# Kernel optimization log

Measured on AMD Instinct MI355X. Metric: run time of the kernel, lower is better.

## Reference

```python
import jax, jax.numpy as jnp
import numpy as np

E = 16   # n_experts
K = 4    # top_k
NEG = jnp.float32(-1e20)


def _swiglu(x, w1, w2, w3):
    # bias-free SwiGLU expert: (swish(x@w1) * (x@w2)) @ w3
    a = x @ w1
    return (a * jax.nn.sigmoid(a) * (x @ w2)) @ w3


def setup_inputs() -> dict:
    key = jax.random.key(0)
    ks = jax.random.split(key, 9)
    B, S, D, H = 32, 512, 512, 1365  # H = D*2*4//3
    s = 0.02  # weight init scale to keep activations sane
    return {
        "x": jax.random.normal(ks[0], (B, S, D), jnp.float32),
        "gate_w": jax.random.normal(ks[1], (D, E), jnp.float32) * s,
        "routing_bias": jnp.zeros((E,), jnp.float32),
        "w1": jax.random.normal(ks[2], (E, D, H), jnp.float32) * s,
        "w2": jax.random.normal(ks[3], (E, D, H), jnp.float32) * s,
        "w3": jax.random.normal(ks[4], (E, H, D), jnp.float32) * s,
        "sw1": jax.random.normal(ks[5], (D, H), jnp.float32) * s,
        "sw2": jax.random.normal(ks[6], (D, H), jnp.float32) * s,
        "sw3": jax.random.normal(ks[7], (H, D), jnp.float32) * s,
    }


def reference(x, gate_w, routing_bias, w1, w2, w3, sw1, sw2, sw3):
    # gate logits + aux-free load-balancing bias  [B,S,E]
    gate_out = x @ gate_w + routing_bias
    top_v, top_i = jax.lax.top_k(gate_out, K)
    # chosen[b,s,e] = 1 if expert e is in the top-k for token (b,s)
    chosen = jax.nn.one_hot(top_i, E, dtype=x.dtype).sum(axis=-2)
    # scatter top-k values onto a -1e20 background, then softmax over experts
    masked = jnp.where(chosen > 0, gate_out, NEG)
    probs = jax.nn.softmax(masked, axis=-1)
    weights = probs * chosen  # zero outside the chosen set (matches torch mask)
    # shared expert runs on all tokens
    out = _swiglu(x, sw1, sw2, sw3)
    # per-expert SwiGLU, weighted-combined (loop over fixed small E)
    for e in range(E):
        out = out + _swiglu(x, w1[e], w2[e], w3[e]) * weights[..., e:e + 1]
    return out
```

## Files before the change

### kernel.cpp

```cpp
#include <hip/hip_runtime.h>

#define NT    16384
#define DDIM  512
#define HDIM  1365
#define HPAD  1408
#define NEXP  16
#define BK    64
#define MAXTILES 336
#define MAXSLOTS 86016

typedef unsigned short u16;
typedef unsigned int   u32;
typedef __attribute__((ext_vector_type(8))) __bf16 bf16x8;
typedef __attribute__((ext_vector_type(4))) float  f32x4;
typedef __attribute__((address_space(3))) void lds_void;
typedef __attribute__((address_space(1))) void glb_void;

__device__ __forceinline__ u16 f2bf(float f) {
  union { float f; u32 u; } v; v.f = f;
  u32 u = v.u;
  u += 0x7fffu + ((u >> 16) & 1u);
  return (u16)(u >> 16);
}

__device__ __forceinline__ float bf2f(u16 b) {
  union { u32 u; float f; } v; v.u = ((u32)b) << 16;
  return v.f;
}

__device__ __forceinline__ f32x4 mfma16(bf16x8 a, bf16x8 b, f32x4 c) {
  return __builtin_amdgcn_mfma_f32_16x16x32_bf16(a, b, c, 0, 0, 0);
}

__device__ __forceinline__ void gload16(const u16* g, u16* l) {
  __builtin_amdgcn_global_load_lds((const glb_void*)g, (lds_void*)l, 16, 0, 0);
}

__device__ __forceinline__ bf16x8 lds_frag(const u16* base, int row, int e0) {
  int b = ((row << 7) + (e0 << 1)) ^ ((row & 7) << 4);
  return *(const bf16x8*)((const char*)base + b);
}

__device__ __forceinline__ int swz_n(int bid, int n) {
  int q = n >> 3, r = n & 7;
  int xcd = bid & 7, j = bid >> 3;
  return (xcd < r ? xcd * (q + 1) : r * (q + 1) + (xcd - r) * q) + j;
}

__global__ void transpose12_kernel(const float* __restrict__ w1, const float* __restrict__ w2,
                                   const float* __restrict__ sw1, const float* __restrict__ sw2,
                                   u16* __restrict__ w1t, u16* __restrict__ w2t,
                                   u16* __restrict__ sw1t, u16* __restrict__ sw2t) {
  __shared__ float tile[32][65];
  int z = blockIdx.z;
  const float* in; u16* out;
  if (z < 16)      { in = w1 + (size_t)z * DDIM * HDIM;        out = w1t + (size_t)z * HPAD * DDIM; }
  else if (z < 32) { in = w2 + (size_t)(z - 16) * DDIM * HDIM; out = w2t + (size_t)(z - 16) * HPAD * DDIM; }
  else if (z == 32){ in = sw1; out = sw1t; }
  else             { in = sw2; out = sw2t; }
  int h0 = blockIdx.x * 32, d0 = blockIdx.y * 64;
  int tx = threadIdx.x, ty = threadIdx.y;
  int h = h0 + tx;
#pragma unroll
  for (int r = 0; r < 8; ++r) {
    int d = d0 + ty + r * 8;
    float v = (h < HDIM) ? in[(size_t)d * HDIM + h] : 0.f;
    tile[tx][ty + r * 8] = v;
  }
  __syncthreads();
#pragma unroll
  for (int r = 0; r < 4; ++r) {
    int hh = h0 + ty + r * 8;
    u32 lo = f2bf(tile[ty + r * 8][2 * tx]);
    u32 hi = f2bf(tile[ty + r * 8][2 * tx + 1]);
    ((u32*)&out[(size_t)hh * DDIM + d0])[tx] = lo | (hi << 16);
  }
}

__global__ void transpose3_kernel(const float* __restrict__ w3, const float* __restrict__ sw3,
                                  u16* __restrict__ w3t, u16* __restrict__ sw3t) {
  __shared__ float tile[32][65];
  int z = blockIdx.z;
  const float* in = (z < 16) ? (w3 + (size_t)z * HDIM * DDIM) : sw3;
  u16* out = (z < 16) ? (w3t + (size_t)z * DDIM * HPAD) : sw3t;
  int h0 = blockIdx.x * 64, d0 = blockIdx.y * 32;
  int tx = threadIdx.x, ty = threadIdx.y;
  int d = d0 + tx;
#pragma unroll
  for (int r = 0; r < 8; ++r) {
    int h = h0 + ty + r * 8;
    float v = (h < HDIM) ? in[(size_t)h * DDIM + d] : 0.f;
    tile[tx][ty + r * 8] = v;
  }
  __syncthreads();
#pragma unroll
  for (int r = 0; r < 4; ++r) {
    int dd = d0 + ty + r * 8;
    u32 lo = f2bf(tile[ty + r * 8][2 * tx]);
    u32 hi = f2bf(tile[ty + r * 8][2 * tx + 1]);
    ((u32*)&out[(size_t)dd * HPAD + h0])[tx] = lo | (hi << 16);
  }
}

__global__ __launch_bounds__(512) void routing_kernel(
    const float* __restrict__ x, const float* __restrict__ gw,
    const float* __restrict__ rbias, u16* __restrict__ x_bf,
    int* __restrict__ top_e, float* __restrict__ top_w) {
  __shared__ float gwp[NEXP * DDIM];
  int tid = threadIdx.x;
  for (int i = tid; i < NEXP * DDIM; i += 512) {
    int d = i >> 4, e = i & 15;
    gwp[e * DDIM + ((d & 7) << 6) + (d >> 3)] = gw[i];
  }
  __syncthreads();
  int w = tid >> 6, lane = tid & 63;
  int t = blockIdx.x * 8 + w;
  const float* xr = x + (size_t)t * DDIM + lane * 8;
  float4 xa = ((const float4*)xr)[0], xb = ((const float4*)xr)[1];
  float xv[8] = {xa.x, xa.y, xa.z, xa.w, xb.x, xb.y, xb.z, xb.w};
  u16 r[8];
#pragma unroll
  for (int k = 0; k < 8; ++k) r[k] = f2bf(xv[k]);
  *(uint4*)&x_bf[(size_t)t * DDIM + lane * 8] = *(const uint4*)r;
  float acc[NEXP];
#pragma unroll
  for (int e = 0; e < NEXP; ++e) {
    const float* ge = gwp + e * DDIM + lane;
    float s = 0.f;
#pragma unroll
    for (int k = 0; k < 8; ++k) s += xv[k] * ge[k << 6];
#pragma unroll
    for (int off = 32; off; off >>= 1) s += __shfl_xor(s, off);
    acc[e] = s + rbias[e];
  }
  if (lane == 0) {
    int sel[4]; float sv[4];
    unsigned used = 0;
#pragma unroll
    for (int i = 0; i < 4; ++i) {
      float best = -1e30f; int bi = 0;
#pragma unroll
      for (int e = 0; e < NEXP; ++e) {
        bool ok = !((used >> e) & 1u) && acc[e] > best;
        best = ok ? acc[e] : best;
        bi   = ok ? e : bi;
      }
      used |= 1u << bi; sel[i] = bi; sv[i] = best;
    }
    float m = sv[0];
    float ex[4]; float s = 0.f;
#pragma unroll
    for (int i = 0; i < 4; ++i) { ex[i] = __expf(sv[i] - m); s += ex[i]; }
    float inv = 1.f / s;
#pragma unroll
    for (int i = 0; i < 4; ++i) {
      top_e[t * 4 + i] = sel[i];
      top_w[t * 4 + i] = ex[i] * inv;
    }
  }
}

__global__ __launch_bounds__(1024) void rank_kernel(const int* __restrict__ top_e,
                                                    int* __restrict__ counts,
                                                    int* __restrict__ top_pos) {
  __shared__ int hist[NEXP], base[NEXP];
  int tid = threadIdx.x;
  int t = blockIdx.x * 1024 + tid;
  if (tid < NEXP) hist[tid] = 0;
  __syncthreads();
  int e4[4], r4[4];
#pragma unroll
  for (int i = 0; i < 4; ++i) {
    e4[i] = top_e[t * 4 + i];
    r4[i] = atomicAdd(&hist[e4[i]], 1);
  }
  __syncthreads();
  if (tid < NEXP) base[tid] = atomicAdd(&counts[tid], hist[tid]);
  __syncthreads();
#pragma unroll
  for (int i = 0; i < 4; ++i) top_pos[t * 4 + i] = base[e4[i]] + r4[i];
}

__global__ __launch_bounds__(256) void finish_kernel(
    const int* __restrict__ counts, const int* __restrict__ top_e,
    const float* __restrict__ top_w, const int* __restrict__ top_pos,
    int* __restrict__ slot_off, int* __restrict__ ntiles, int2* __restrict__ desc,
    int* __restrict__ tok_pad, float* __restrict__ w_pad, int* __restrict__ pos_list) {
  __shared__ int s_off[17], s_tb[17], s_nt[17], s_cnt[17];
  int tid = threadIdx.x;
  if (tid == 0) {
    int off = 0, td = 0;
    for (int e = 0; e < 17; ++e) {
      int c = (e == 16) ? NT : counts[e];
      s_cnt[e] = c; s_off[e] = off;
      int nt = (c + 255) >> 8;
      s_nt[e] = nt; s_tb[e] = td;
      td += nt; off += nt * 256;
    }
    if (blockIdx.x == 0) {
      for (int e = 0; e < 17; ++e) slot_off[e] = s_off[e];
      slot_off[17] = off;
      *ntiles = td;
    }
  }
  __syncthreads();
  if (blockIdx.x == 0) {
    for (int e = 0; e < 17; ++e)
      for (int i = tid; i < s_nt[e]; i += 256)
        desc[s_tb[e] + i] = make_int2(e, s_off[e] + i * 256);
  } else if (blockIdx.x == 1) {
    for (int e = 0; e < 16; ++e) {
      int c = s_cnt[e], padded = s_nt[e] * 256;
      for (int i = c + tid; i < padded; i += 256) {
        tok_pad[s_off[e] + i] = 0;
        w_pad[s_off[e] + i] = 0.f;
      }
    }
  }
  int t = blockIdx.x * 256 + tid;
#pragma unroll
  for (int i = 0; i < 4; ++i) {
    int e = top_e[t * 4 + i];
    int slot = s_off[e] + top_pos[t * 4 + i];
    tok_pad[slot] = t;
    w_pad[slot] = top_w[t * 4 + i];
    pos_list[t * 4 + i] = slot;
  }
  int sh = s_off[16] + t;
  tok_pad[sh] = t;
  w_pad[sh] = 1.f;
}

__global__ __launch_bounds__(512, 2) void gemm1_kernel(
    const u16* __restrict__ x_bf, const u16* __restrict__ w1t, const u16* __restrict__ w2t,
    const u16* __restrict__ sw1t, const u16* __restrict__ sw2t,
    const int* __restrict__ ntiles, const int2* __restrict__ desc,
    const int* __restrict__ tok_pad, u16* __restrict__ h, int lo, int ntc) {
  int wk = swz_n(blockIdx.x, ntc * 11);
  int tloc = wk / 11, hblk = wk - tloc * 11;
  int ti = (lo >> 8) + tloc;
  if (ti >= *ntiles) return;
  int2 de = desc[ti];
  int e = de.x, m0 = de.y;
  int n0h = hblk * 128;
  const u16* W1 = (e == 16) ? sw1t : (w1t + (size_t)e * HPAD * DDIM);
  const u16* W2 = (e == 16) ? sw2t : (w2t + (size_t)e * HPAD * DDIM);

  __shared__ u16 smem[65536];
  u16* As = smem;
  u16* Bs = smem + 32768;

  int tid = threadIdx.x, w = tid >> 6, lane = tid & 63;
  int wm = w >> 2, wn = w & 3, lr = lane & 15, lk = lane >> 4;

  const u16* ags[4]; const u16* bgs[4];
#pragma unroll
  for (int l = 0; l < 4; ++l) {
    int idx = l * 512 + tid;
    int row = idx >> 3, sl = idx & 7;
    int ce = ((sl ^ (row & 7)) << 3);
    ags[l] = x_bf + (size_t)tok_pad[m0 + row] * DDIM + ce;
    int grp = row >> 4;
    const u16* Wsrc = (grp & 1) ? W2 : W1;
    int hrow = n0h + ((grp >> 1) << 4) + (row & 15);
    bgs[l] = Wsrc + (size_t)hrow * DDIM + ce;
  }

  auto stage = [&](int kt, int buf) {
    int k0 = kt * BK;
#pragma unroll
    for (int l = 0; l < 4; ++l) {
      int db = buf * 16384 + l * 4096 + (w << 9);
      gload16(ags[l] + k0, As + db);
      gload16(bgs[l] + k0, Bs + db);
    }
  };

  f32x4 acc[8][4] = {};

  stage(0, 0);
  stage(1, 1);

  for (int t = 0; t < DDIM / BK; ++t) {
    int cur = t & 1;
    asm volatile("s_waitcnt vmcnt(8)" ::: "memory");
    __builtin_amdgcn_s_barrier();
    const u16* Ab = As + cur * 16384;
    const u16* Bb = Bs + cur * 16384;
#pragma unroll
    for (int kf = 0; kf < 2; ++kf) {
      int e0 = kf * 32 + lk * 8;
      bf16x8 bfr[4];
#pragma unroll
      for (int nf = 0; nf < 4; ++nf)
        bfr[nf] = lds_frag(Bb, wn * 64 + nf * 16 + lr, e0);
#pragma unroll
      for (int mf = 0; mf < 8; ++mf) {
        bf16x8 a = lds_frag(Ab, wm * 128 + mf * 16 + lr, e0);
#pragma unroll
        for (int nf = 0; nf < 4; ++nf)
          acc[mf][nf] = mfma16(a, bfr[nf], acc[mf][nf]);
      }
    }
    __builtin_amdgcn_s_barrier();
    int tn = (t + 2 < DDIM / BK) ? t + 2 : DDIM / BK - 1;
    stage(tn, cur);
  }
  asm volatile("s_waitcnt vmcnt(0)" ::: "memory");
  __builtin_amdgcn_s_barrier();

  u16* hs = smem;
#pragma unroll
  for (int mf = 0; mf < 8; ++mf)
#pragma unroll
    for (int hc = 0; hc < 2; ++hc)
#pragma unroll
      for (int j = 0; j < 4; ++j) {
        float g = acc[mf][hc * 2][j], u = acc[mf][hc * 2 + 1][j];
        float hv = g * u / (1.f + __expf(-g));
        int row = wm * 128 + mf * 16 + lk * 4 + j;
        int col = (wn * 2 + hc) * 16 + lr;
        hs[((row << 7) + col) ^ ((row & 7) << 3)] = f2bf(hv);
      }
  __syncthreads();
#pragma unroll
  for (int i = 0; i < 8; ++i) {
    int idx = (i * 512 + tid) * 8;
    int row = idx >> 7, col = idx & 127;
    *(uint4*)&h[(size_t)(m0 - lo + row) * HPAD + n0h + col] =
        *(uint4*)&hs[idx ^ ((row & 7) << 3)];
  }
}

template <bool YMODE>
__global__ __launch_bounds__(256, 3) void gemm2_kernel(
    const u16* __restrict__ h, const u16* __restrict__ w3t, const u16* __restrict__ sw3t,
    const int* __restrict__ ntiles, const int2* __restrict__ desc,
    const int* __restrict__ tok_pad, const float* __restrict__ w_pad,
    u16* __restrict__ y, float* __restrict__ out, int lo, int ntc) {
  int wk = swz_n(blockIdx.x, ntc * 8);
  int tloc = wk >> 3, sub = (wk >> 2) & 1, dblk = wk & 3;
  int ti = (lo >> 8) + tloc;
  if (ti >= *ntiles) return;
  int2 de = desc[ti];
  int e = de.x, m0 = de.y + sub * 128;
  int n0 = dblk * 128;
  const u16* W3 = (e == 16) ? sw3t : (w3t + (size_t)e * DDIM * HPAD);

  __shared__ u16 smem[16384];
  __shared__ float swl[128];
  u16* hs = smem;
  u16* ws3 = smem + 8192;

  int tid = threadIdx.x, w = tid >> 6, lane = tid & 63;
  int wm = w >> 1, wn = w & 1, lr = lane & 15, lk = lane >> 4;

  if (tid < 128) swl[tid] = w_pad[m0 + tid];

  const u16* ags[4]; const u16* bgs[4];
  int ce = (((lane & 7) ^ ((lane >> 3) & 7)) << 3);
#pragma unroll
  for (int p = 0; p < 4; ++p) {
    int r = w * 32 + p * 8 + (lane >> 3);
    ags[p] = h + (size_t)(m0 - lo + r) * HPAD + ce;
    bgs[p] = W3 + (size_t)(n0 + r) * HPAD + ce;
  }

  f32x4 acc[4][4] = {};

  for (int ks = 0; ks < HPAD / BK; ++ks) {
    int k0 = ks * BK;
#pragma unroll
    for (int p = 0; p < 4; ++p) {
      gload16(ags[p] + k0, hs + ((w * 32 + p * 8) << 6));
      gload16(bgs[p] + k0, ws3 + ((w * 32 + p * 8) << 6));
    }
    __syncthreads();
#pragma unroll
    for (int kf = 0; kf < 2; ++kf) {
      int e0 = kf * 32 + lk * 8;
      bf16x8 bfr[4];
#pragma unroll
      for (int nf = 0; nf < 4; ++nf)
        bfr[nf] = lds_frag(ws3, wn * 64 + nf * 16 + lr, e0);
#pragma unroll
      for (int mf = 0; mf < 4; ++mf) {
        bf16x8 a = lds_frag(hs, wm * 64 + mf * 16 + lr, e0);
#pragma unroll
        for (int nf = 0; nf < 4; ++nf)
          acc[mf][nf] = mfma16(a, bfr[nf], acc[mf][nf]);
      }
    }
    __syncthreads();
  }

  if constexpr (YMODE) {
    u16* ys = smem;
#pragma unroll
    for (int mf = 0; mf < 4; ++mf)
#pragma unroll
      for (int j = 0; j < 4; ++j) {
        int row = wm * 64 + mf * 16 + lk * 4 + j;
        float wv = swl[row];
#pragma unroll
        for (int nf = 0; nf < 4; ++nf)
          ys[((row << 7) + wn * 64 + nf * 16 + lr) ^ ((row & 7) << 3)] =
              f2bf(acc[mf][nf][j] * wv);
      }
    __syncthreads();
#pragma unroll
    for (int i = 0; i < 8; ++i) {
      int idx = (i * 256 + tid) * 8;
      int row = idx >> 7, col = idx & 127;
      *(uint4*)&y[(size_t)(m0 + row) * DDIM + n0 + col] =
          *(uint4*)&smem[idx ^ ((row & 7) << 3)];
    }
  } else {
#pragma unroll
    for (int mf = 0; mf < 4; ++mf)
#pragma unroll
      for (int j = 0; j < 4; ++j) {
        int row = wm * 64 + mf * 16 + lk * 4 + j;
        float wv = swl[row];
        float* orow = out + (size_t)tok_pad[m0 + row] * DDIM + n0;
#pragma unroll
        for (int nf = 0; nf < 4; ++nf)
          atomicAdd(&orow[wn * 64 + nf * 16 + lr], acc[mf][nf][j] * wv);
      }
  }
}

__global__ void reduce_kernel(const u16* __restrict__ y, const int* __restrict__ pos_list,
                              const int* __restrict__ slot_off, float* __restrict__ out) {
  int t = blockIdx.x;
  int c = threadIdx.x;
  int4 pl = ((const int4*)pos_list)[t];
  int sh = slot_off[16] + t;
  ushort4 a = ((const ushort4*)(y + (size_t)sh * DDIM))[c];
  ushort4 b = ((const ushort4*)(y + (size_t)pl.x * DDIM))[c];
  ushort4 d = ((const ushort4*)(y + (size_t)pl.y * DDIM))[c];
  ushort4 e = ((const ushort4*)(y + (size_t)pl.z * DDIM))[c];
  ushort4 f = ((const ushort4*)(y + (size_t)pl.w * DDIM))[c];
  float4 s;
  s.x = bf2f(a.x) + bf2f(b.x) + bf2f(d.x) + bf2f(e.x) + bf2f(f.x);
  s.y = bf2f(a.y) + bf2f(b.y) + bf2f(d.y) + bf2f(e.y) + bf2f(f.y);
  s.z = bf2f(a.z) + bf2f(b.z) + bf2f(d.z) + bf2f(e.z) + bf2f(f.z);
  s.w = bf2f(a.w) + bf2f(b.w) + bf2f(d.w) + bf2f(e.w) + bf2f(f.w);
  ((float4*)(out + (size_t)t * DDIM))[c] = s;
}

extern "C" void kernel_launch(void* const* d_in, const int* in_sizes, int n_in,
                              void* d_out, int out_size, void* d_ws, size_t ws_size,
                              hipStream_t stream) {
  const float* x      = (const float*)d_in[0];
  const float* gate_w = (const float*)d_in[1];
  const float* rbias  = (const float*)d_in[2];
  const float* w1     = (const float*)d_in[3];
  const float* w2     = (const float*)d_in[4];
  const float* w3     = (const float*)d_in[5];
  const float* sw1    = (const float*)d_in[6];
  const float* sw2    = (const float*)d_in[7];
  const float* sw3    = (const float*)d_in[8];
  float* out = (float*)d_out;

  char* ws = (char*)d_ws;
  size_t off = 0;
  auto alloc = [&](size_t bytes) -> char* {
    char* p = ws + off;
    off += (bytes + 255) & ~(size_t)255;
    return p;
  };
  u16* x_bf  = (u16*)alloc((size_t)NT * DDIM * 2);
  u16* w1t   = (u16*)alloc((size_t)NEXP * HPAD * DDIM * 2);
  u16* w2t   = (u16*)alloc((size_t)NEXP * HPAD * DDIM * 2);
  u16* w3t   = (u16*)alloc((size_t)NEXP * DDIM * HPAD * 2);
  u16* sw1t  = (u16*)alloc((size_t)HPAD * DDIM * 2);
  u16* sw2t  = (u16*)alloc((size_t)HPAD * DDIM * 2);
  u16* sw3t  = (u16*)alloc((size_t)DDIM * HPAD * 2);
  int*   counts   = (int*)alloc(64 * 4);
  int*   top_e    = (int*)alloc((size_t)NT * 4 * 4);
  float* top_w    = (float*)alloc((size_t)NT * 4 * 4);
  int*   top_pos  = (int*)alloc((size_t)NT * 4 * 4);
  int*   slot_off = (int*)alloc(32 * 4);
  int*   ntiles   = (int*)alloc(256);
  int2*  desc     = (int2*)alloc((size_t)MAXTILES * 8);
  int*   tok_pad  = (int*)alloc((size_t)MAXSLOTS * 4);
  float* w_pad    = (float*)alloc((size_t)MAXSLOTS * 4);
  int*   pos_list = (int*)alloc((size_t)NT * 4 * 4);
  size_t y_off = off;
  u16* y = (u16*)alloc((size_t)MAXSLOTS * DDIM * 2);
  size_t h_off_y = off;
  (void)in_sizes; (void)n_in; (void)ws_size;

  const size_t per_row = (size_t)HPAD * 2;
  bool ymode;
  size_t h_off, rows_avail;
  size_t avail_y = (ws_size > h_off_y) ? (ws_size - h_off_y) : 0;
  if (avail_y / per_row >= 10752) {
    ymode = true; h_off = h_off_y; rows_avail = avail_y / per_row;
  } else {
    ymode = false; h_off = y_off;
    size_t avail_a = (ws_size > y_off) ? (ws_size - y_off) : 0;
    rows_avail = avail_a / per_row;
  }
  int CS;
  if (rows_avail >= (size_t)MAXSLOTS) CS = MAXSLOTS;
  else {
    CS = (int)((rows_avail / 2048) * 2048);
    if (CS < 2048) CS = (int)((rows_avail / 256) * 256);
    if (CS < 256) CS = 256;
  }
  int NCH = (MAXSLOTS + CS - 1) / CS;
  u16* h = (u16*)(ws + h_off);

  hipMemsetAsync(counts, 0, 64 * 4, stream);
  if (!ymode) hipMemsetAsync(out, 0, (size_t)out_size * 4, stream);

  dim3 tb(32, 8);
  transpose12_kernel<<<dim3(HPAD / 32, DDIM / 64, 34), tb, 0, stream>>>(
      w1, w2, sw1, sw2, w1t, w2t, sw1t, sw2t);
  transpose3_kernel<<<dim3(HPAD / 64, DDIM / 32, 17), tb, 0, stream>>>(
      w3, sw3, w3t, sw3t);

  routing_kernel<<<NT / 8, 512, 0, stream>>>(x, gate_w, rbias, x_bf, top_e, top_w);
  rank_kernel<<<NT / 1024, 1024, 0, stream>>>(top_e, counts, top_pos);
  finish_kernel<<<NT / 256, 256, 0, stream>>>(counts, top_e, top_w, top_pos,
                                              slot_off, ntiles, desc,
                                              tok_pad, w_pad, pos_list);

  for (int c = 0; c < NCH; ++c) {
    int lo = c * CS;
    int ntc = (MAXSLOTS - lo < CS ? MAXSLOTS - lo : CS) >> 8;
    gemm1_kernel<<<ntc * 11, 512, 0, stream>>>(
        x_bf, w1t, w2t, sw1t, sw2t, ntiles, desc, tok_pad, h, lo, ntc);
    if (ymode)
      gemm2_kernel<true><<<ntc * 8, 256, 0, stream>>>(
          h, w3t, sw3t, ntiles, desc, tok_pad, w_pad, y, out, lo, ntc);
    else
      gemm2_kernel<false><<<ntc * 8, 256, 0, stream>>>(
          h, w3t, sw3t, ntiles, desc, tok_pad, w_pad, y, out, lo, ntc);
  }
  if (ymode) reduce_kernel<<<NT, 128, 0, stream>>>(y, pos_list, slot_off, out);
}
```

Baseline: 666.1 us.

## Restructure gemm1 main loop into 8-wave ping-pong schedule with split K halves

Rewrites the gemm1 K-loop so each 64-wide K tile is split into two 32-wide halves with separate LDS layouts and swizzle. Global loads for the next stages are interleaved between four MFMA clusters fenced by barriers and sched_barriers, with s_setprio raised around the MFMA blocks. The goal is finer overlap of global-to-LDS traffic and LDS fragment reads with matrix math. Dropping the occupancy hint of 2 blocks per CU frees the register budget for the extra fragment registers, at the cost of lower occupancy. The many added barriers also add synchronization overhead.

```diff
diff --git a/kernel.cpp b/kernel.cpp
--- a/kernel.cpp
+++ b/kernel.cpp
@@ -231,7 +231,7 @@
   w_pad[sh] = 1.f;
 }
 
-__global__ __launch_bounds__(512, 2) void gemm1_kernel(
+__global__ __launch_bounds__(512) void gemm1_kernel(
     const u16* __restrict__ x_bf, const u16* __restrict__ w1t, const u16* __restrict__ w2t,
     const u16* __restrict__ sw1t, const u16* __restrict__ sw2t,
     const int* __restrict__ ntiles, const int2* __restrict__ desc,
@@ -253,61 +253,130 @@
   int tid = threadIdx.x, w = tid >> 6, lane = tid & 63;
   int wm = w >> 2, wn = w & 3, lr = lane & 15, lk = lane >> 4;
 
-  const u16* ags[4]; const u16* bgs[4];
-#pragma unroll
-  for (int l = 0; l < 4; ++l) {
-    int idx = l * 512 + tid;
-    int row = idx >> 3, sl = idx & 7;
-    int ce = ((sl ^ (row & 7)) << 3);
-    ags[l] = x_bf + (size_t)tok_pad[m0 + row] * DDIM + ce;
+  const u16* ag[2]; const u16* bg[2]; int doff[2];
+#pragma unroll
+  for (int l = 0; l < 2; ++l) {
+    int cidx = l * 512 + tid;
+    int row = cidx >> 2, c = cidx & 3;
+    int sc = c ^ ((row >> 1) & 3);
+    ag[l] = x_bf + (size_t)tok_pad[m0 + row] * DDIM + sc * 8;
     int grp = row >> 4;
     const u16* Wsrc = (grp & 1) ? W2 : W1;
     int hrow = n0h + ((grp >> 1) << 4) + (row & 15);
-    bgs[l] = Wsrc + (size_t)hrow * DDIM + ce;
-  }
-
-  auto stage = [&](int kt, int buf) {
-    int k0 = kt * BK;
-#pragma unroll
-    for (int l = 0; l < 4; ++l) {
-      int db = buf * 16384 + l * 4096 + (w << 9);
-      gload16(ags[l] + k0, As + db);
-      gload16(bgs[l] + k0, Bs + db);
-    }
+    bg[l] = Wsrc + (size_t)hrow * DDIM + sc * 8;
+    doff[l] = cidx * 8;
+  }
+
+  auto stageA = [&](int kt, int kf, int buf) {
+#pragma unroll
+    for (int l = 0; l < 2; ++l)
+      gload16(ag[l] + kt * 64 + kf * 32, As + buf * 16384 + kf * 8192 + doff[l]);
   };
+  auto stageB = [&](int kt, int kf, int buf) {
+#pragma unroll
+    for (int l = 0; l < 2; ++l)
+      gload16(bg[l] + kt * 64 + kf * 32, Bs + buf * 16384 + kf * 8192 + doff[l]);
+  };
+  auto fragA = [&](int buf, int kf, int row) {
+    return *(const bf16x8*)(As + buf * 16384 + kf * 8192 + row * 32 +
+                            ((lk ^ ((row >> 1) & 3)) << 3));
+  };
+  auto fragB = [&](int buf, int kf, int row) {
+    return *(const bf16x8*)(Bs + buf * 16384 + kf * 8192 + row * 32 +
+                            ((lk ^ ((row >> 1) & 3)) << 3));
+  };
 
   f32x4 acc[8][4] = {};
-
-  stage(0, 0);
-  stage(1, 1);
-
-  for (int t = 0; t < DDIM / BK; ++t) {
-    int cur = t & 1;
+  bf16x8 bfr[4], afr[4];
+
+  const int NTK = DDIM / BK;
+  stageA(0, 0, 0); stageB(0, 0, 0);
+  stageA(0, 1, 0); stageB(0, 1, 0);
+  stageA(1, 0, 1); stageB(1, 0, 1);
+  asm volatile("s_waitcnt vmcnt(8)" ::: "memory");
+  __builtin_amdgcn_sched_barrier(0);
+  __builtin_amdgcn_s_barrier();
+  __builtin_amdgcn_sched_barrier(0);
+
+  for (int t = 0; t < NTK; ++t) {
+    int buf = t & 1;
+    int t1 = (t + 1 < NTK) ? t + 1 : NTK - 1;
+    int t2 = (t + 2 < NTK) ? t + 2 : NTK - 1;
+#pragma unroll
+    for (int nf = 0; nf < 4; ++nf) bfr[nf] = fragB(buf, 0, wn * 64 + nf * 16 + lr);
+#pragma unroll
+    for (int mf = 0; mf < 4; ++mf) afr[mf] = fragA(buf, 0, wm * 128 + mf * 16 + lr);
+    stageA(t1, 1, buf ^ 1);
+    __builtin_amdgcn_sched_barrier(0);
+    __builtin_amdgcn_s_barrier();
+    __builtin_amdgcn_sched_barrier(0);
+    __builtin_amdgcn_s_setprio(1);
+#pragma unroll
+    for (int mf = 0; mf < 4; ++mf)
+#pragma unroll
+      for (int nf = 0; nf < 4; ++nf)
+        acc[mf][nf] = mfma16(afr[mf], bfr[nf], acc[mf][nf]);
+    __builtin_amdgcn_s_setprio(0);
+    __builtin_amdgcn_sched_barrier(0);
+    __builtin_amdgcn_s_barrier();
+    __builtin_amdgcn_sched_barrier(0);
+#pragma unroll
+    for (int mf = 0; mf < 4; ++mf) afr[mf] = fragA(buf, 0, wm * 128 + (mf + 4) * 16 + lr);
+    stageB(t1, 1, buf ^ 1);
     asm volatile("s_waitcnt vmcnt(8)" ::: "memory");
-    __builtin_amdgcn_s_barrier();
-    const u16* Ab = As + cur * 16384;
-    const u16* Bb = Bs + cur * 16384;
-#pragma unroll
-    for (int kf = 0; kf < 2; ++kf) {
-      int e0 = kf * 32 + lk * 8;
-      bf16x8 bfr[4];
+    __builtin_amdgcn_sched_barrier(0);
+    __builtin_amdgcn_s_barrier();
+    __builtin_amdgcn_sched_barrier(0);
+    __builtin_amdgcn_s_setprio(1);
+#pragma unroll
+    for (int mf = 0; mf < 4; ++mf)
 #pragma unroll
       for (int nf = 0; nf < 4; ++nf)
-        bfr[nf] = lds_frag(Bb, wn * 64 + nf * 16 + lr, e0);
-#pragma unroll
-      for (int mf = 0; mf < 8; ++mf) {
-        bf16x8 a = lds_frag(Ab, wm * 128 + mf * 16 + lr, e0);
-#pragma unroll
-        for (int nf = 0; nf < 4; ++nf)
-          acc[mf][nf] = mfma16(a, bfr[nf], acc[mf][nf]);
-      }
-    }
-    __builtin_amdgcn_s_barrier();
-    int tn = (t + 2 < DDIM / BK) ? t + 2 : DDIM / BK - 1;
-    stage(tn, cur);
+        acc[mf + 4][nf] = mfma16(afr[mf], bfr[nf], acc[mf + 4][nf]);
+    __builtin_amdgcn_s_setprio(0);
+    __builtin_amdgcn_sched_barrier(0);
+    __builtin_amdgcn_s_barrier();
+    __builtin_amdgcn_sched_barrier(0);
+#pragma unroll
+    for (int nf = 0; nf < 4; ++nf) bfr[nf] = fragB(buf, 1, wn * 64 + nf * 16 + lr);
+#pragma unroll
+    for (int mf = 0; mf < 4; ++mf) afr[mf] = fragA(buf, 1, wm * 128 + mf * 16 + lr);
+    stageA(t2, 0, buf);
+    __builtin_amdgcn_sched_barrier(0);
+    __builtin_amdgcn_s_barrier();
+    __builtin_amdgcn_sched_barrier(0);
+    __builtin_amdgcn_s_setprio(1);
+#pragma unroll
+    for (int mf = 0; mf < 4; ++mf)
+#pragma unroll
+      for (int nf = 0; nf < 4; ++nf)
+        acc[mf][nf] = mfma16(afr[mf], bfr[nf], acc[mf][nf]);
+    __builtin_amdgcn_s_setprio(0);
+    __builtin_amdgcn_sched_barrier(0);
+    __builtin_amdgcn_s_barrier();
+    __builtin_amdgcn_sched_barrier(0);
+#pragma unroll
+    for (int mf = 0; mf < 4; ++mf) afr[mf] = fragA(buf, 1, wm * 128 + (mf + 4) * 16 + lr);
+    stageB(t2, 0, buf);
+    asm volatile("s_waitcnt vmcnt(8)" ::: "memory");
+    __builtin_amdgcn_sched_barrier(0);
+    __builtin_amdgcn_s_barrier();
+    __builtin_amdgcn_sched_barrier(0);
+    __builtin_amdgcn_s_setprio(1);
+#pragma unroll
+    for (int mf = 0; mf < 4; ++mf)
+#pragma unroll
+      for (int nf = 0; nf < 4; ++nf)
+        acc[mf + 4][nf] = mfma16(afr[mf], bfr[nf], acc[mf + 4][nf]);
+    __builtin_amdgcn_s_setprio(0);
+    __builtin_amdgcn_sched_barrier(0);
+    __builtin_amdgcn_s_barrier();
+    __builtin_amdgcn_sched_barrier(0);
   }
   asm volatile("s_waitcnt vmcnt(0)" ::: "memory");
+  __builtin_amdgcn_sched_barrier(0);
   __builtin_amdgcn_s_barrier();
+  __builtin_amdgcn_sched_barrier(0);
 
   u16* hs = smem;
 #pragma unroll
```

New measurement: 676.8 us. About the same (+1.6%).
